# Performance work log

Measured on AMD Instinct MI355X. Metric: run time of the kernel, lower is better.

## Reference

```python
import jax, jax.numpy as jnp
import numpy as np
import math
from itertools import combinations_with_replacement

D_KEY, D_VAL, P = 32, 64, 2
ALPHA = 1.0 / (math.factorial(P) * D_KEY ** (P / 2))  # 1/(p! * d_key^(p/2))
B, H, S = 1, 8, 512


def _make_M_C():
    # M_p: unique monomial index tuples i_1 <= ... <= i_p, shape [m_p, p]
    M = np.array(list(combinations_with_replacement(range(D_KEY), P)), dtype=np.int32)
    m_p = M.shape[0]
    counts = np.zeros((m_p, D_KEY), dtype=np.int64)
    for j in range(P):
        counts[np.arange(m_p), M[:, j]] += 1
    logfac_counts = np.vectorize(lambda v: math.lgamma(v + 1.0))(counts).sum(-1)
    C = np.round(np.exp(math.lgamma(P + 1.0) - logfac_counts)).astype(np.float32)
    return M, C


def setup_inputs() -> dict:
    key = jax.random.key(0)
    kq, kk, kv = jax.random.split(key, 3)
    M, C = _make_M_C()
    return {
        "Q": jax.random.normal(kq, (B, H, S, D_KEY), dtype=jnp.float32),
        "K": jax.random.normal(kk, (B, H, S, D_KEY), dtype=jnp.float32),
        "V": jax.random.normal(kv, (B, H, S, D_VAL), dtype=jnp.float32),
        "M": jnp.asarray(M),
        "C": jnp.asarray(C),
        "continue_prev": 0,
    }


def reference(Q, K, V, M, C, continue_prev):
    # Monomial features: Phi[b,h,s,m] = prod_j X[b,h,s,M[m,j]]
    Phi_Q = jnp.prod(Q[..., M], axis=-1)  # [B,H,S,m]
    Phi_K = jnp.prod(K[..., M], axis=-1)  # [B,H,S,m]
    # Causal prefix-sum of the Phi_K (x) V outer-product state
    H_S = jnp.cumsum(Phi_K[..., None] * V[..., None, :], axis=-3) * ALPHA  # [B,H,S,m,d_val]
    H_Z = jnp.cumsum(Phi_K, axis=-2) * ALPHA                                # [B,H,S,m] (d=1 squeezed)
    # continue_prev is False (0): no carried state to add.
    Y_S = jnp.einsum('m,bhsm,bhsmd->bhsd', C, Phi_Q, H_S)  # [B,H,S,d_val]
    Y_Z = jnp.einsum('m,bhsm,bhsm->bhs', C, Phi_Q, H_Z)[..., None]  # [B,H,S,1]
    return Y_S, Y_Z
```

## Files before the change

### kernel.cpp

```cpp
#include <hip/hip_runtime.h>


typedef __attribute__((ext_vector_type(8))) short short8;
typedef __attribute__((ext_vector_type(4))) float floatx4;

constexpr int H_ = 8, S_ = 512, DK = 32, DV = 64;
constexpr float ALPHA = 1.0f / 64.0f;

__device__ __forceinline__ unsigned short f2bf(float x) {
    unsigned int u = __float_as_uint(x);
    u += 0x7FFFu + ((u >> 16) & 1u);
    return (unsigned short)(u >> 16);
}
__device__ __forceinline__ float bf2f(unsigned short h) {
    return __uint_as_float(((unsigned int)h) << 16);
}
__device__ __forceinline__ void load_split8(const float* p, short8& hi, short8& lo) {
    float4 a = *(const float4*)p;
    float4 b = *(const float4*)(p + 4);
    float f[8] = {a.x, a.y, a.z, a.w, b.x, b.y, b.z, b.w};
    #pragma unroll
    for (int j = 0; j < 8; ++j) {
        unsigned short h = f2bf(f[j]);
        hi[j] = (short)h;
        lo[j] = (short)f2bf(f[j] - bf2f(h));
    }
}

__global__ __launch_bounds__(512) void taylor_fused(
    const float* __restrict__ Qg, const float* __restrict__ Kg,
    const float* __restrict__ Vg, float* __restrict__ out)
{
    const int t = threadIdx.x;
    const int c = t >> 6;
    const int l = t & 63;
    const int h = blockIdx.x & 7;
    const int qt = 15 - (blockIdx.x >> 3);
    const int qbase = qt * 32;
    const int nc = (qt >> 1) + 1;
    const int g = l >> 4, r15 = l & 15;

    __shared__ alignas(16) char Ssm[8 * 4096];
    __shared__ alignas(16) char Racc[8 * 8192];
    __shared__ float Zb[8][32];

    floatx4 acc[2][4] = {};
    float zacc[2] = {0.f, 0.f};

    if (c < nc) {
        const bool last = (c == nc - 1);

        short8 qBh[2], qBl[2];
        #pragma unroll
        for (int qtile = 0; qtile < 2; ++qtile)
            load_split8(Qg + (size_t)(h * S_ + qbase + qtile * 16 + r15) * DK + g * 8,
                        qBh[qtile], qBl[qtile]);

        short8 vB[2][4];
        #pragma unroll
        for (int kc = 0; kc < 2; ++kc)
            #pragma unroll
            for (int dtile = 0; dtile < 4; ++dtile) {
                const float* vp = Vg + (size_t)(h * S_ + c * 64 + kc * 32 + g * 8) * DV
                                     + dtile * 16 + r15;
                #pragma unroll
                for (int j = 0; j < 8; ++j)
                    vB[kc][dtile][j] = (short)f2bf(vp[(size_t)j * DV]);
            }

        char* ssmW = Ssm + c * 4096;

        #pragma unroll
        for (int ktile = 0; ktile < 4; ++ktile) {
            short8 kAh, kAl;
            load_split8(Kg + (size_t)(h * S_ + c * 64 + ktile * 16 + r15) * DK + g * 8,
                        kAh, kAl);
            #pragma unroll
            for (int qtile = 0; qtile < 2; ++qtile) {
                floatx4 cc_ = {0.f, 0.f, 0.f, 0.f};
                cc_ = __builtin_amdgcn_mfma_f32_16x16x32_bf16(kAh, qBh[qtile], cc_, 0, 0, 0);
                cc_ = __builtin_amdgcn_mfma_f32_16x16x32_bf16(kAh, qBl[qtile], cc_, 0, 0, 0);
                cc_ = __builtin_amdgcn_mfma_f32_16x16x32_bf16(kAl, qBh[qtile], cc_, 0, 0, 0);
                const int qg = qbase + qtile * 16 + r15;
                const int kb = c * 64 + ktile * 16 + g * 4;
                float s[4];
                #pragma unroll
                for (int rr = 0; rr < 4; ++rr) {
                    float sv = cc_[rr] * cc_[rr] * ALPHA;
                    if (last && (kb + rr > qg)) sv = 0.f;
                    s[rr] = sv;
                }
                zacc[qtile] += (s[0] + s[1]) + (s[2] + s[3]);
                unsigned int p0 = (unsigned int)f2bf(s[0]) | ((unsigned int)f2bf(s[1]) << 16);
                unsigned int p1 = (unsigned int)f2bf(s[2]) | ((unsigned int)f2bf(s[3]) << 16);
                const int qrow = qtile * 16 + r15;
                const int k0 = ktile * 16 + g * 4;
                const int byte = qrow * 128 + (((k0 >> 3) ^ (qrow & 7)) << 4) + ((k0 & 7) * 2);
                *(unsigned int*)(ssmW + byte)     = p0;
                *(unsigned int*)(ssmW + byte + 4) = p1;
            }
        }

        #pragma unroll
        for (int kc = 0; kc < 2; ++kc) {
            short8 sA[2];
            #pragma unroll
            for (int qtile = 0; qtile < 2; ++qtile) {
                const int qrow = qtile * 16 + r15;
                const int g16 = kc * 4 + g;
                sA[qtile] = *(const short8*)(ssmW + qrow * 128 + ((g16 ^ (qrow & 7)) << 4));
            }
            #pragma unroll
            for (int dtile = 0; dtile < 4; ++dtile) {
                acc[0][dtile] = __builtin_amdgcn_mfma_f32_16x16x32_bf16(sA[0], vB[kc][dtile], acc[0][dtile], 0, 0, 0);
                acc[1][dtile] = __builtin_amdgcn_mfma_f32_16x16x32_bf16(sA[1], vB[kc][dtile], acc[1][dtile], 0, 0, 0);
            }
        }

        #pragma unroll
        for (int qtile = 0; qtile < 2; ++qtile) {
            float z = zacc[qtile];
            z += __shfl_xor(z, 16);
            z += __shfl_xor(z, 32);
            zacc[qtile] = z;
        }
    }

    {
        char* rb = Racc + c * 8192 + l * 128;
        #pragma unroll
        for (int f = 0; f < 8; ++f) {
            floatx4 a = acc[f >> 2][f & 3];
            *(float4*)(rb + ((f ^ (l & 7)) << 4)) = make_float4(a[0], a[1], a[2], a[3]);
        }
        if (l < 32) Zb[c][l] = (l < 16) ? zacc[0] : zacc[1];
    }
    __syncthreads();

    {
        float4 sum = make_float4(0.f, 0.f, 0.f, 0.f);
        #pragma unroll
        for (int cw = 0; cw < 8; ++cw) {
            float4 v = *(const float4*)(Racc + cw * 8192 + l * 128 + ((c ^ (l & 7)) << 4));
            sum.x += v.x; sum.y += v.y; sum.z += v.z; sum.w += v.w;
        }
        const int qtile = c >> 2, dtile = c & 3;
        const int d = dtile * 16 + r15;
        float sv[4] = {sum.x, sum.y, sum.z, sum.w};
        #pragma unroll
        for (int rr = 0; rr < 4; ++rr) {
            int q = qbase + qtile * 16 + g * 4 + rr;
            out[(size_t)(h * S_ + q) * DV + d] = sv[rr];
        }
    }
    if (t < 32) {
        float z = 0.f;
        #pragma unroll
        for (int cw = 0; cw < 8; ++cw) z += Zb[cw][t];
        out[(size_t)(H_ * S_ * DV) + h * S_ + qbase + t] = z;
    }
}

extern "C" void kernel_launch(void* const* d_in, const int* in_sizes, int n_in,
                              void* d_out, int out_size, void* d_ws, size_t ws_size,
                              hipStream_t stream) {
    const float* Q = (const float*)d_in[0];
    const float* K = (const float*)d_in[1];
    const float* V = (const float*)d_in[2];
    float* out = (float*)d_out;

    taylor_fused<<<128, 512, 0, stream>>>(Q, K, V, out);
}
```

Before: 11.72 us.

## Hoist all global loads up front, use packed bf16 converts, simplify reduction layout

```diff
diff --git a/kernel.cpp b/kernel.cpp
--- a/kernel.cpp
+++ b/kernel.cpp
@@ -1,4 +1,5 @@
 #include <hip/hip_runtime.h>
+#include <hip/hip_bf16.h>
 
 
 typedef __attribute__((ext_vector_type(8))) short short8;
@@ -7,27 +8,36 @@
 constexpr int H_ = 8, S_ = 512, DK = 32, DV = 64;
 constexpr float ALPHA = 1.0f / 64.0f;
 
-__device__ __forceinline__ unsigned short f2bf(float x) {
-    unsigned int u = __float_as_uint(x);
-    u += 0x7FFFu + ((u >> 16) & 1u);
-    return (unsigned short)(u >> 16);
-}
-__device__ __forceinline__ float bf2f(unsigned short h) {
-    return __uint_as_float(((unsigned int)h) << 16);
-}
-__device__ __forceinline__ void load_split8(const float* p, short8& hi, short8& lo) {
-    float4 a = *(const float4*)p;
-    float4 b = *(const float4*)(p + 4);
+__device__ __forceinline__ unsigned int pk_bf16(float a, float b) {
+    __hip_bfloat162 h = __float22bfloat162_rn(make_float2(a, b));
+    union { __hip_bfloat162 h2; unsigned int u; } cvt;
+    cvt.h2 = h;
+    return cvt.u;
+}
+__device__ __forceinline__ void split8_cvt(float4 a, float4 b, short8& hi, short8& lo) {
     float f[8] = {a.x, a.y, a.z, a.w, b.x, b.y, b.z, b.w};
+    unsigned int hp[4];
+    hp[0] = pk_bf16(f[0], f[1]); hp[1] = pk_bf16(f[2], f[3]);
+    hp[2] = pk_bf16(f[4], f[5]); hp[3] = pk_bf16(f[6], f[7]);
+    float lo_f[8];
     #pragma unroll
-    for (int j = 0; j < 8; ++j) {
-        unsigned short h = f2bf(f[j]);
-        hi[j] = (short)h;
-        lo[j] = (short)f2bf(f[j] - bf2f(h));
-    }
-}
-
-__global__ __launch_bounds__(512) void taylor_fused(
+    for (int p = 0; p < 4; ++p) {
+        float he = __uint_as_float(hp[p] << 16);
+        float ho = __uint_as_float(hp[p] & 0xFFFF0000u);
+        lo_f[2 * p]     = f[2 * p]     - he;
+        lo_f[2 * p + 1] = f[2 * p + 1] - ho;
+    }
+    unsigned int lp[4];
+    lp[0] = pk_bf16(lo_f[0], lo_f[1]); lp[1] = pk_bf16(lo_f[2], lo_f[3]);
+    lp[2] = pk_bf16(lo_f[4], lo_f[5]); lp[3] = pk_bf16(lo_f[6], lo_f[7]);
+    #pragma unroll
+    for (int p = 0; p < 4; ++p) {
+        hi[2 * p] = (short)(hp[p] & 0xFFFF); hi[2 * p + 1] = (short)(hp[p] >> 16);
+        lo[2 * p] = (short)(lp[p] & 0xFFFF); lo[2 * p + 1] = (short)(lp[p] >> 16);
+    }
+}
+
+__global__ __launch_bounds__(512) void taylor_fused_v6(
     const float* __restrict__ Qg, const float* __restrict__ Kg,
     const float* __restrict__ Vg, float* __restrict__ out)
 {
@@ -41,7 +51,7 @@
     const int g = l >> 4, r15 = l & 15;
 
     __shared__ alignas(16) char Ssm[8 * 4096];
-    __shared__ alignas(16) char Racc[8 * 8192];
+    __shared__ alignas(16) float4 Racc[8][8][64];
     __shared__ float Zb[8][32];
 
     floatx4 acc[2][4] = {};
@@ -50,13 +60,21 @@
     if (c < nc) {
         const bool last = (c == nc - 1);
 
-        short8 qBh[2], qBl[2];
-        #pragma unroll
-        for (int qtile = 0; qtile < 2; ++qtile)
-            load_split8(Qg + (size_t)(h * S_ + qbase + qtile * 16 + r15) * DK + g * 8,
-                        qBh[qtile], qBl[qtile]);
-
-        short8 vB[2][4];
+        float4 qraw[2][2];
+        #pragma unroll
+        for (int qtile = 0; qtile < 2; ++qtile) {
+            const float* qp = Qg + (size_t)(h * S_ + qbase + qtile * 16 + r15) * DK + g * 8;
+            qraw[qtile][0] = *(const float4*)qp;
+            qraw[qtile][1] = *(const float4*)(qp + 4);
+        }
+        float4 kraw[4][2];
+        #pragma unroll
+        for (int ktile = 0; ktile < 4; ++ktile) {
+            const float* kp = Kg + (size_t)(h * S_ + c * 64 + ktile * 16 + r15) * DK + g * 8;
+            kraw[ktile][0] = *(const float4*)kp;
+            kraw[ktile][1] = *(const float4*)(kp + 4);
+        }
+        float vraw[2][4][8];
         #pragma unroll
         for (int kc = 0; kc < 2; ++kc)
             #pragma unroll
@@ -65,16 +83,20 @@
                                      + dtile * 16 + r15;
                 #pragma unroll
                 for (int j = 0; j < 8; ++j)
-                    vB[kc][dtile][j] = (short)f2bf(vp[(size_t)j * DV]);
-            }
+                    vraw[kc][dtile][j] = vp[(size_t)j * DV];
+            }
+
+        short8 qBh[2], qBl[2];
+        #pragma unroll
+        for (int qtile = 0; qtile < 2; ++qtile)
+            split8_cvt(qraw[qtile][0], qraw[qtile][1], qBh[qtile], qBl[qtile]);
 
         char* ssmW = Ssm + c * 4096;
 
         #pragma unroll
         for (int ktile = 0; ktile < 4; ++ktile) {
             short8 kAh, kAl;
-            load_split8(Kg + (size_t)(h * S_ + c * 64 + ktile * 16 + r15) * DK + g * 8,
-                        kAh, kAl);
+            split8_cvt(kraw[ktile][0], kraw[ktile][1], kAh, kAl);
             #pragma unroll
             for (int qtile = 0; qtile < 2; ++qtile) {
                 floatx4 cc_ = {0.f, 0.f, 0.f, 0.f};
@@ -91,8 +113,8 @@
                     s[rr] = sv;
                 }
                 zacc[qtile] += (s[0] + s[1]) + (s[2] + s[3]);
-                unsigned int p0 = (unsigned int)f2bf(s[0]) | ((unsigned int)f2bf(s[1]) << 16);
-                unsigned int p1 = (unsigned int)f2bf(s[2]) | ((unsigned int)f2bf(s[3]) << 16);
+                unsigned int p0 = pk_bf16(s[0], s[1]);
+                unsigned int p1 = pk_bf16(s[2], s[3]);
                 const int qrow = qtile * 16 + r15;
                 const int k0 = ktile * 16 + g * 4;
                 const int byte = qrow * 128 + (((k0 >> 3) ^ (qrow & 7)) << 4) + ((k0 & 7) * 2);
@@ -101,6 +123,19 @@
             }
         }
 
+        short8 vB[2][4];
+        #pragma unroll
+        for (int kc = 0; kc < 2; ++kc)
+            #pragma unroll
+            for (int dtile = 0; dtile < 4; ++dtile) {
+                #pragma unroll
+                for (int p = 0; p < 4; ++p) {
+                    unsigned int pk = pk_bf16(vraw[kc][dtile][2 * p], vraw[kc][dtile][2 * p + 1]);
+                    vB[kc][dtile][2 * p]     = (short)(pk & 0xFFFF);
+                    vB[kc][dtile][2 * p + 1] = (short)(pk >> 16);
+                }
+            }
+
         #pragma unroll
         for (int kc = 0; kc < 2; ++kc) {
             short8 sA[2];
@@ -127,11 +162,10 @@
     }
 
     {
-        char* rb = Racc + c * 8192 + l * 128;
         #pragma unroll
         for (int f = 0; f < 8; ++f) {
             floatx4 a = acc[f >> 2][f & 3];
-            *(float4*)(rb + ((f ^ (l & 7)) << 4)) = make_float4(a[0], a[1], a[2], a[3]);
+            Racc[c][f][l] = make_float4(a[0], a[1], a[2], a[3]);
         }
         if (l < 32) Zb[c][l] = (l < 16) ? zacc[0] : zacc[1];
     }
@@ -141,7 +175,7 @@
         float4 sum = make_float4(0.f, 0.f, 0.f, 0.f);
         #pragma unroll
         for (int cw = 0; cw < 8; ++cw) {
-            float4 v = *(const float4*)(Racc + cw * 8192 + l * 128 + ((c ^ (l & 7)) << 4));
+            float4 v = Racc[cw][c][l];
             sum.x += v.x; sum.y += v.y; sum.z += v.z; sum.w += v.w;
         }
         const int qtile = c >> 2, dtile = c & 3;
@@ -169,5 +203,5 @@
     const float* V = (const float*)d_in[2];
     float* out = (float*)d_out;
 
-    taylor_fused<<<128, 512, 0, stream>>>(Q, K, V, out);
-}
+    taylor_fused_v6<<<128, 512, 0, stream>>>(Q, K, V, out);
+}
```

After: 11.29 us. 3.7% less time.
